# Optimization experiments

Hardware: AMD Instinct MI355X
Metric: run time of the kernel (lower is better)

Reference implementation:

```python
import jax, jax.numpy as jnp
import numpy as np

ALPHA = 0.2      # LeakyReLU negative slope (hardcoded in StateNetwork: GAT(..., 0.2, 1))
MASK_FILL = 9e-15  # value used for non-edges BEFORE softmax (not -inf, per original code)

N_ENT = 4096     # len(vocab_kge): number of KG entities / GAT nodes
EMB = 64         # embedding_size == gat_emb_size
NHID = 3         # hardcoded in StateNetwork: GAT(gat_emb_size, 3, ...)
BATCH = 4        # number of graphs in graph_rep


def setup_inputs() -> dict:
    key = jax.random.key(0)
    k_adj, k_emb, k_W, k_a, k_fw, k_fb = jax.random.split(key, 6)
    adj = jax.random.randint(k_adj, (BATCH, N_ENT, N_ENT), 0, 2, dtype=jnp.int32)
    ent_emb = jax.random.normal(k_emb, (N_ENT, EMB), dtype=jnp.float32)
    W = jax.random.normal(k_W, (EMB, NHID), dtype=jnp.float32)
    a = jax.random.normal(k_a, (2 * NHID, 1), dtype=jnp.float32)
    fc1_w = jax.random.normal(k_fw, (100, N_ENT * NHID), dtype=jnp.float32) * 0.02
    fc1_b = jax.random.normal(k_fb, (100,), dtype=jnp.float32)
    return {"adj": adj, "ent_emb": ent_emb, "W": W, "a": a, "fc1_w": fc1_w, "fc1_b": fc1_b}


def reference(adj, ent_emb, W, a, fc1_w, fc1_b):
    # GAT layer over the shared entity-embedding node features (same for all graphs).
    h = ent_emb @ W                                   # [N, F]
    F_out = h.shape[1]
    # Pairwise concat score decomposes: e[i,j] = leakyrelu(a1.h_i + a2.h_j)
    src = h @ a[:F_out]                                # [N, 1]
    dst = h @ a[F_out:]                                # [N, 1]
    e = jax.nn.leaky_relu(src + dst.T, negative_slope=ALPHA)   # [N, N]
    # Masked softmax with 9e-15 fill (faithful to torch.where(adj>0, e, 9e-15))
    att = jnp.where(adj > 0, e[None, :, :], jnp.float32(MASK_FILL))  # [B, N, N]
    att = jax.nn.softmax(att, axis=-1)
    h_prime = jnp.einsum('bij,jf->bif', att, h)        # [B, N, F]
    x = jax.nn.elu(h_prime)                            # concat=True -> ELU
    x = x.reshape(adj.shape[0], -1)                    # [B, N*F]
    return x @ fc1_w.T + fc1_b                         # [B, 100]
```

## Files before the change

### kernel.cpp

```cpp
#include <hip/hip_runtime.h>
#include <math.h>

#define N_ENT 4096
#define BATCH 4
#define NHID  3
#define EMB   64
#define ALPHA 0.2f
#define MASK_FILL 9e-15f
#define LOG2E 1.4426950408889634f
#define MASKP (MASK_FILL * LOG2E)

#if defined(__has_builtin)
#  if __has_builtin(__builtin_amdgcn_exp2f)
#    define EXP2F(x) __builtin_amdgcn_exp2f(x)
#  else
#    define EXP2F(x) exp2f(x)
#  endif
#else
#  define EXP2F(x) exp2f(x)
#endif

typedef int v4i __attribute__((ext_vector_type(4)));

__device__ __forceinline__ v4i nt_load(const v4i* p) {
    return __builtin_nontemporal_load(p);
}

__global__ __launch_bounds__(256) void prep_kernel(
    const float* __restrict__ emb, const float* __restrict__ W,
    const float* __restrict__ a,
    float* __restrict__ h0G, float* __restrict__ h1G, float* __restrict__ h2G,
    float* __restrict__ dstG, float* __restrict__ srcG)
{
    int j = blockIdx.x * 256 + threadIdx.x;
    if (j >= N_ENT) return;
    const float* er = emb + (size_t)j * EMB;
    float h0 = 0.f, h1 = 0.f, h2 = 0.f;
    #pragma unroll
    for (int e = 0; e < EMB; ++e) {
        float v = er[e];
        h0 += v * W[e * 3 + 0];
        h1 += v * W[e * 3 + 1];
        h2 += v * W[e * 3 + 2];
    }
    h0G[j] = h0; h1G[j] = h1; h2G[j] = h2;
    srcG[j] = (h0 * a[0] + h1 * a[1] + h2 * a[2]) * LOG2E;
    dstG[j] = (h0 * a[3] + h1 * a[4] + h2 * a[5]) * LOG2E;
}

__global__ __launch_bounds__(1024, 4) void gat_row_kernel(
    const int* __restrict__ adj,
    const float* __restrict__ h0G, const float* __restrict__ h1G,
    const float* __restrict__ h2G, const float* __restrict__ dstG,
    const float* __restrict__ srcG, float* __restrict__ xG)
{
    __shared__ float dstL[N_ENT];
    __shared__ float h0L[N_ENT];
    __shared__ float h1L[N_ENT];
    __shared__ float h2L[N_ENT];
    __shared__ float maxdL[16];

    int tid  = threadIdx.x;
    int lane = tid & 63;
    int wid  = tid >> 6;

    float md = -3.4e38f;
    #pragma unroll
    for (int t = tid; t < N_ENT; t += 1024) {
        float dv = dstG[t];
        dstL[t] = dv;
        md = fmaxf(md, dv);
        h0L[t] = h0G[t];
        h1L[t] = h1G[t];
        h2L[t] = h2G[t];
    }
    #pragma unroll
    for (int off = 32; off; off >>= 1) md = fmaxf(md, __shfl_xor(md, off, 64));
    if (lane == 0) maxdL[wid] = md;
    __syncthreads();
    float maxd = maxdL[0];
    #pragma unroll
    for (int t = 1; t < 16; ++t) maxd = fmaxf(maxd, maxdL[t]);

    int i = blockIdx.x * 16 + wid;

    float srcp = srcG[i];
    float tt = srcp + maxd;
    float M  = fmaxf(fmaxf(tt, ALPHA * tt), (float)MASKP);
    float s0 = srcp - M, s1 = ALPHA * srcp - M;
    float C  = EXP2F((float)MASKP - M);

    const v4i* p0 = (const v4i*)(adj + ((size_t)0 * N_ENT + i) * N_ENT);
    const v4i* p1 = (const v4i*)(adj + ((size_t)1 * N_ENT + i) * N_ENT);
    const v4i* p2 = (const v4i*)(adj + ((size_t)2 * N_ENT + i) * N_ENT);
    const v4i* p3 = (const v4i*)(adj + ((size_t)3 * N_ENT + i) * N_ENT);

    v4i cur0 = nt_load(p0 + lane),      cur1 = nt_load(p1 + lane);
    v4i cur2 = nt_load(p2 + lane),      cur3 = nt_load(p3 + lane);
    v4i nxt0 = nt_load(p0 + 64 + lane), nxt1 = nt_load(p1 + 64 + lane);
    v4i nxt2 = nt_load(p2 + 64 + lane), nxt3 = nt_load(p3 + 64 + lane);

    float l0 = 0.f, n00 = 0.f, n01 = 0.f, n02 = 0.f;
    float l1 = 0.f, n10 = 0.f, n11 = 0.f, n12 = 0.f;
    float l2 = 0.f, n20 = 0.f, n21 = 0.f, n22 = 0.f;
    float l3 = 0.f, n30 = 0.f, n31 = 0.f, n32 = 0.f;

    #pragma unroll 1
    for (int c = 0; c < 16; ++c) {
        v4i a0v = cur0, a1v = cur1, a2v = cur2, a3v = cur3;
        cur0 = nxt0; cur1 = nxt1; cur2 = nxt2; cur3 = nxt3;
        int cn = (c + 2) & 15;
        nxt0 = nt_load(p0 + cn * 64 + lane);
        nxt1 = nt_load(p1 + cn * 64 + lane);
        nxt2 = nt_load(p2 + cn * 64 + lane);
        nxt3 = nt_load(p3 + cn * 64 + lane);

        int jb = (c * 64 + lane) * 4;
        float4 d4 = *(const float4*)&dstL[jb];
        float4 h0 = *(const float4*)&h0L[jb];
        float4 h1 = *(const float4*)&h1L[jb];
        float4 h2 = *(const float4*)&h2L[jb];

        float g0 = EXP2F(fmaxf(s0 + d4.x, fmaf(ALPHA, d4.x, s1)));
        float g1 = EXP2F(fmaxf(s0 + d4.y, fmaf(ALPHA, d4.y, s1)));
        float g2 = EXP2F(fmaxf(s0 + d4.z, fmaf(ALPHA, d4.z, s1)));
        float g3 = EXP2F(fmaxf(s0 + d4.w, fmaf(ALPHA, d4.w, s1)));

        {
            float w0 = a0v.x > 0 ? g0 : C, w1 = a0v.y > 0 ? g1 : C;
            float w2 = a0v.z > 0 ? g2 : C, w3 = a0v.w > 0 ? g3 : C;
            l0 += (w0 + w1) + (w2 + w3);
            n00 = fmaf(w0, h0.x, fmaf(w1, h0.y, fmaf(w2, h0.z, fmaf(w3, h0.w, n00))));
            n01 = fmaf(w0, h1.x, fmaf(w1, h1.y, fmaf(w2, h1.z, fmaf(w3, h1.w, n01))));
            n02 = fmaf(w0, h2.x, fmaf(w1, h2.y, fmaf(w2, h2.z, fmaf(w3, h2.w, n02))));
        }
        {
            float w0 = a1v.x > 0 ? g0 : C, w1 = a1v.y > 0 ? g1 : C;
            float w2 = a1v.z > 0 ? g2 : C, w3 = a1v.w > 0 ? g3 : C;
            l1 += (w0 + w1) + (w2 + w3);
            n10 = fmaf(w0, h0.x, fmaf(w1, h0.y, fmaf(w2, h0.z, fmaf(w3, h0.w, n10))));
            n11 = fmaf(w0, h1.x, fmaf(w1, h1.y, fmaf(w2, h1.z, fmaf(w3, h1.w, n11))));
            n12 = fmaf(w0, h2.x, fmaf(w1, h2.y, fmaf(w2, h2.z, fmaf(w3, h2.w, n12))));
        }
        {
            float w0 = a2v.x > 0 ? g0 : C, w1 = a2v.y > 0 ? g1 : C;
            float w2 = a2v.z > 0 ? g2 : C, w3 = a2v.w > 0 ? g3 : C;
            l2 += (w0 + w1) + (w2 + w3);
            n20 = fmaf(w0, h0.x, fmaf(w1, h0.y, fmaf(w2, h0.z, fmaf(w3, h0.w, n20))));
            n21 = fmaf(w0, h1.x, fmaf(w1, h1.y, fmaf(w2, h1.z, fmaf(w3, h1.w, n21))));
            n22 = fmaf(w0, h2.x, fmaf(w1, h2.y, fmaf(w2, h2.z, fmaf(w3, h2.w, n22))));
        }
        {
            float w0 = a3v.x > 0 ? g0 : C, w1 = a3v.y > 0 ? g1 : C;
            float w2 = a3v.z > 0 ? g2 : C, w3 = a3v.w > 0 ? g3 : C;
            l3 += (w0 + w1) + (w2 + w3);
            n30 = fmaf(w0, h0.x, fmaf(w1, h0.y, fmaf(w2, h0.z, fmaf(w3, h0.w, n30))));
            n31 = fmaf(w0, h1.x, fmaf(w1, h1.y, fmaf(w2, h1.z, fmaf(w3, h1.w, n31))));
            n32 = fmaf(w0, h2.x, fmaf(w1, h2.y, fmaf(w2, h2.z, fmaf(w3, h2.w, n32))));
        }
    }

    #pragma unroll
    for (int off = 32; off; off >>= 1) {
        l0  += __shfl_xor(l0,  off, 64);
        n00 += __shfl_xor(n00, off, 64);
        n01 += __shfl_xor(n01, off, 64);
        n02 += __shfl_xor(n02, off, 64);
        l1  += __shfl_xor(l1,  off, 64);
        n10 += __shfl_xor(n10, off, 64);
        n11 += __shfl_xor(n11, off, 64);
        n12 += __shfl_xor(n12, off, 64);
        l2  += __shfl_xor(l2,  off, 64);
        n20 += __shfl_xor(n20, off, 64);
        n21 += __shfl_xor(n21, off, 64);
        n22 += __shfl_xor(n22, off, 64);
        l3  += __shfl_xor(l3,  off, 64);
        n30 += __shfl_xor(n30, off, 64);
        n31 += __shfl_xor(n31, off, 64);
        n32 += __shfl_xor(n32, off, 64);
    }

    if (lane == 0) {
        float inv, v0, v1, v2;
        float* xp;
        inv = 1.f / l0; v0 = n00*inv; v1 = n01*inv; v2 = n02*inv;
        xp = xG + ((size_t)0 * N_ENT + i) * 3;
        xp[0] = v0 > 0.f ? v0 : expm1f(v0);
        xp[1] = v1 > 0.f ? v1 : expm1f(v1);
        xp[2] = v2 > 0.f ? v2 : expm1f(v2);
        inv = 1.f / l1; v0 = n10*inv; v1 = n11*inv; v2 = n12*inv;
        xp = xG + ((size_t)1 * N_ENT + i) * 3;
        xp[0] = v0 > 0.f ? v0 : expm1f(v0);
        xp[1] = v1 > 0.f ? v1 : expm1f(v1);
        xp[2] = v2 > 0.f ? v2 : expm1f(v2);
        inv = 1.f / l2; v0 = n20*inv; v1 = n21*inv; v2 = n22*inv;
        xp = xG + ((size_t)2 * N_ENT + i) * 3;
        xp[0] = v0 > 0.f ? v0 : expm1f(v0);
        xp[1] = v1 > 0.f ? v1 : expm1f(v1);
        xp[2] = v2 > 0.f ? v2 : expm1f(v2);
        inv = 1.f / l3; v0 = n30*inv; v1 = n31*inv; v2 = n32*inv;
        xp = xG + ((size_t)3 * N_ENT + i) * 3;
        xp[0] = v0 > 0.f ? v0 : expm1f(v0);
        xp[1] = v1 > 0.f ? v1 : expm1f(v1);
        xp[2] = v2 > 0.f ? v2 : expm1f(v2);
    }
}

__global__ __launch_bounds__(256) void fc_kernel(
    const float* __restrict__ xG, const float* __restrict__ w,
    const float* __restrict__ bias, float* __restrict__ out)
{
    int k   = blockIdx.x;
    int tid = threadIdx.x;
    const float4* wr = (const float4*)(w + (size_t)k * (N_ENT * NHID));
    const float4* x0 = (const float4*)(xG + 0 * (N_ENT * NHID));
    const float4* x1 = (const float4*)(xG + 1 * (N_ENT * NHID));
    const float4* x2 = (const float4*)(xG + 2 * (N_ENT * NHID));
    const float4* x3 = (const float4*)(xG + 3 * (N_ENT * NHID));

    float acc0 = 0.f, acc1 = 0.f, acc2 = 0.f, acc3 = 0.f;
    for (int t = tid; t < (N_ENT * NHID / 4); t += 256) {
        float4 wv = wr[t];
        float4 xv;
        xv = x0[t]; acc0 += wv.x*xv.x + wv.y*xv.y + wv.z*xv.z + wv.w*xv.w;
        xv = x1[t]; acc1 += wv.x*xv.x + wv.y*xv.y + wv.z*xv.z + wv.w*xv.w;
        xv = x2[t]; acc2 += wv.x*xv.x + wv.y*xv.y + wv.z*xv.z + wv.w*xv.w;
        xv = x3[t]; acc3 += wv.x*xv.x + wv.y*xv.y + wv.z*xv.z + wv.w*xv.w;
    }

    #pragma unroll
    for (int off = 32; off; off >>= 1) {
        acc0 += __shfl_xor(acc0, off, 64);
        acc1 += __shfl_xor(acc1, off, 64);
        acc2 += __shfl_xor(acc2, off, 64);
        acc3 += __shfl_xor(acc3, off, 64);
    }

    __shared__ float red[4][4];
    int lane = tid & 63, wv_ = tid >> 6;
    if (lane == 0) {
        red[wv_][0] = acc0; red[wv_][1] = acc1;
        red[wv_][2] = acc2; red[wv_][3] = acc3;
    }
    __syncthreads();
    if (tid < 4) {
        float s = red[0][tid] + red[1][tid] + red[2][tid] + red[3][tid] + bias[k];
        out[tid * 100 + k] = s;
    }
}

extern "C" void kernel_launch(void* const* d_in, const int* in_sizes, int n_in,
                              void* d_out, int out_size, void* d_ws, size_t ws_size,
                              hipStream_t stream)
{
    const int*   adj  = (const int*)d_in[0];
    const float* emb  = (const float*)d_in[1];
    const float* W    = (const float*)d_in[2];
    const float* a    = (const float*)d_in[3];
    const float* fc1w = (const float*)d_in[4];
    const float* fc1b = (const float*)d_in[5];
    float* out = (float*)d_out;

    float* ws   = (float*)d_ws;
    float* h0G  = ws;
    float* h1G  = ws + 4096;
    float* h2G  = ws + 8192;
    float* dstG = ws + 12288;
    float* srcG = ws + 16384;
    float* xG   = ws + 20480;

    prep_kernel<<<N_ENT / 256, 256, 0, stream>>>(emb, W, a, h0G, h1G, h2G, dstG, srcG);
    gat_row_kernel<<<N_ENT / 16, 1024, 0, stream>>>(adj, h0G, h1G, h2G, dstG, srcG, xG);
    fc_kernel<<<100, 256, 0, stream>>>(xG, fc1w, fc1b, out);
}
```

Baseline: 360.9 us.

## Deepen adjacency prefetch to four stages and halve GAT block size

The GAT row kernel's adjacency streaming is reworked from a two-deep prefetch into a four-deep ring buffer. The 16-chunk loop is now fully unrolled, with no loads issued after chunk 12 instead of wrapping around to redundant loads. Block size is also cut from 1024 to 512 threads (8 rows per block), which doubles the block count so more independent workgroups can overlap memory latency. The cost is more registers per thread and twice the per-block LDS staging of the 64KB node tables, since each block now covers fewer rows.

```diff
diff --git a/kernel.cpp b/kernel.cpp
--- a/kernel.cpp
+++ b/kernel.cpp
@@ -48,7 +48,7 @@
     dstG[j] = (h0 * a[3] + h1 * a[4] + h2 * a[5]) * LOG2E;
 }
 
-__global__ __launch_bounds__(1024, 4) void gat_row_kernel(
+__global__ __launch_bounds__(512, 4) void gat_row_kernel(
     const int* __restrict__ adj,
     const float* __restrict__ h0G, const float* __restrict__ h1G,
     const float* __restrict__ h2G, const float* __restrict__ dstG,
@@ -58,7 +58,7 @@
     __shared__ float h0L[N_ENT];
     __shared__ float h1L[N_ENT];
     __shared__ float h2L[N_ENT];
-    __shared__ float maxdL[16];
+    __shared__ float maxdL[8];
 
     int tid  = threadIdx.x;
     int lane = tid & 63;
@@ -66,7 +66,7 @@
 
     float md = -3.4e38f;
     #pragma unroll
-    for (int t = tid; t < N_ENT; t += 1024) {
+    for (int t = tid; t < N_ENT; t += 512) {
         float dv = dstG[t];
         dstL[t] = dv;
         md = fmaxf(md, dv);
@@ -80,9 +80,9 @@
     __syncthreads();
     float maxd = maxdL[0];
     #pragma unroll
-    for (int t = 1; t < 16; ++t) maxd = fmaxf(maxd, maxdL[t]);
-
-    int i = blockIdx.x * 16 + wid;
+    for (int t = 1; t < 8; ++t) maxd = fmaxf(maxd, maxdL[t]);
+
+    int i = blockIdx.x * 8 + wid;
 
     float srcp = srcG[i];
     float tt = srcp + maxd;
@@ -95,25 +95,31 @@
     const v4i* p2 = (const v4i*)(adj + ((size_t)2 * N_ENT + i) * N_ENT);
     const v4i* p3 = (const v4i*)(adj + ((size_t)3 * N_ENT + i) * N_ENT);
 
-    v4i cur0 = nt_load(p0 + lane),      cur1 = nt_load(p1 + lane);
-    v4i cur2 = nt_load(p2 + lane),      cur3 = nt_load(p3 + lane);
-    v4i nxt0 = nt_load(p0 + 64 + lane), nxt1 = nt_load(p1 + 64 + lane);
-    v4i nxt2 = nt_load(p2 + 64 + lane), nxt3 = nt_load(p3 + 64 + lane);
+    v4i bA[4], bB[4], bC[4], bD[4];
+    #pragma unroll
+    for (int c = 0; c < 4; ++c) {
+        bA[c] = nt_load(p0 + c * 64 + lane);
+        bB[c] = nt_load(p1 + c * 64 + lane);
+        bC[c] = nt_load(p2 + c * 64 + lane);
+        bD[c] = nt_load(p3 + c * 64 + lane);
+    }
 
     float l0 = 0.f, n00 = 0.f, n01 = 0.f, n02 = 0.f;
     float l1 = 0.f, n10 = 0.f, n11 = 0.f, n12 = 0.f;
     float l2 = 0.f, n20 = 0.f, n21 = 0.f, n22 = 0.f;
     float l3 = 0.f, n30 = 0.f, n31 = 0.f, n32 = 0.f;
 
-    #pragma unroll 1
+    #pragma unroll
     for (int c = 0; c < 16; ++c) {
-        v4i a0v = cur0, a1v = cur1, a2v = cur2, a3v = cur3;
-        cur0 = nxt0; cur1 = nxt1; cur2 = nxt2; cur3 = nxt3;
-        int cn = (c + 2) & 15;
-        nxt0 = nt_load(p0 + cn * 64 + lane);
-        nxt1 = nt_load(p1 + cn * 64 + lane);
-        nxt2 = nt_load(p2 + cn * 64 + lane);
-        nxt3 = nt_load(p3 + cn * 64 + lane);
+        int s = c & 3;
+        v4i a0v = bA[s], a1v = bB[s], a2v = bC[s], a3v = bD[s];
+        if (c < 12) {
+            int cn = c + 4;
+            bA[s] = nt_load(p0 + cn * 64 + lane);
+            bB[s] = nt_load(p1 + cn * 64 + lane);
+            bC[s] = nt_load(p2 + cn * 64 + lane);
+            bD[s] = nt_load(p3 + cn * 64 + lane);
+        }
 
         int jb = (c * 64 + lane) * 4;
         float4 d4 = *(const float4*)&dstL[jb];
@@ -270,6 +276,6 @@
     float* xG   = ws + 20480;
 
     prep_kernel<<<N_ENT / 256, 256, 0, stream>>>(emb, W, a, h0G, h1G, h2G, dstG, srcG);
-    gat_row_kernel<<<N_ENT / 16, 1024, 0, stream>>>(adj, h0G, h1G, h2G, dstG, srcG, xG);
+    gat_row_kernel<<<N_ENT / 8, 512, 0, stream>>>(adj, h0G, h1G, h2G, dstG, srcG, xG);
     fc_kernel<<<100, 256, 0, stream>>>(xG, fc1w, fc1b, out);
 }
```

After: 371.8 us. 1.03x slower.
